# Optimization experiments

Hardware: AMD Instinct MI355X
Metric: run time of the kernel (lower is better)

The kernel has to match this reference:

```python
import jax, jax.numpy as jnp
import numpy as np
from jax import lax

B, C_IN, C_OUT, H, W, K, MID = 16, 256, 256, 64, 64, 3, 64
BN_EPS = 1e-5


def setup_inputs() -> dict:
    key = jax.random.key(0)
    ks = jax.random.split(key, 16)
    inp = {
        'x': jax.random.normal(ks[0], (B, C_IN, H, W), dtype=jnp.float32),
        # 4 kernel banks: (4, c2, c1//g, k, k)
        'weight': jax.random.normal(ks[1], (4, C_OUT, C_IN, K, K), dtype=jnp.float32) * 0.05,
        'gamma': jnp.ones((C_OUT,), jnp.float32),
        'beta': jnp.zeros((C_OUT,), jnp.float32),
    }
    # four attention branches: Linear(c, mid, bias=False) -> ReLU -> Linear(mid, 4, bias=True)
    names = ['s', 'c', 'f', 'w']
    for i, n in enumerate(names):
        inp[f'fc_{n}_w1'] = jax.random.normal(ks[2 + 3 * i], (MID, C_IN), dtype=jnp.float32) * 0.05
        inp[f'fc_{n}_w2'] = jax.random.normal(ks[3 + 3 * i], (4, MID), dtype=jnp.float32) * 0.05
        inp[f'fc_{n}_b2'] = jax.random.normal(ks[4 + 3 * i], (4,), dtype=jnp.float32) * 0.05
    return inp


def _branch(pooled, w1, w2, b2):
    # pooled: [B, C]; w1: [MID, C]; w2: [4, MID]
    h = jax.nn.relu(pooled @ w1.T)
    return jax.nn.softmax(h @ w2.T + b2, axis=1)  # [B, 4]


def reference(x, weight, gamma, beta,
              fc_s_w1, fc_s_w2, fc_s_b2,
              fc_c_w1, fc_c_w2, fc_c_b2,
              fc_f_w1, fc_f_w2, fc_f_b2,
              fc_w_w1, fc_w_w2, fc_w_b2):
    b = x.shape[0]
    pooled = jnp.mean(x, axis=(2, 3))  # GAP -> [B, C]
    alpha = (_branch(pooled, fc_s_w1, fc_s_w2, fc_s_b2)
             * _branch(pooled, fc_c_w1, fc_c_w2, fc_c_b2)
             * _branch(pooled, fc_f_w1, fc_f_w2, fc_f_b2)
             * _branch(pooled, fc_w_w1, fc_w_w2, fc_w_b2))  # [B, 4]
    # per-sample dynamic kernels: [B, out_c, in_c, k, k]
    dyn_w = jnp.einsum('bn,noikl->boikl', alpha, weight)

    def conv_one(xi, wi):
        # xi: [C, H, W]; wi: [out_c, in_c, k, k]
        return lax.conv_general_dilated(
            xi[None], wi, window_strides=(1, 1), padding='SAME',
            dimension_numbers=('NCHW', 'OIHW', 'NCHW'))[0]

    out = jax.vmap(conv_one)(x, dyn_w)  # [B, out_c, H, W]

    # BatchNorm2d (training-mode batch statistics)
    mean = jnp.mean(out, axis=(0, 2, 3))
    var = jnp.var(out, axis=(0, 2, 3))
    out = (out - mean[None, :, None, None]) * jax.lax.rsqrt(var + BN_EPS)[None, :, None, None]
    return out * gamma[None, :, None, None] + beta[None, :, None, None]
```

## Files before the change

kernel.cpp:

```cpp
#include <hip/hip_runtime.h>
#include <math.h>

#define BB 16
#define CIN 256
#define COUT 256
#define HH 64
#define WW 64
#define NBANK_STRIDE 589824

typedef short bf16x8 __attribute__((ext_vector_type(8)));
typedef float f32x4 __attribute__((ext_vector_type(4)));

#define WS_XT_OFF 32768
#define WS_DW_OFF 33587200
#define WS_NEED   52461568ULL

static __device__ __forceinline__ short f2bf(float f) {
    union { float f; unsigned u; } v; v.f = f;
    unsigned r = v.u + 0x7FFF + ((v.u >> 16) & 1);
    return (short)(r >> 16);
}

struct AttnParams {
    const float* w1[4];
    const float* w2[4];
    const float* b2[4];
};

__global__ __launch_bounds__(256) void xpose_kernel(const float* __restrict__ x,
                                                    short* __restrict__ xT,
                                                    float* __restrict__ pooled_part,
                                                    float* __restrict__ bn_part) {
    const int ci0 = blockIdx.x * 32;
    const int hg = blockIdx.y;
    const int h0 = hg * 4;
    const int b = blockIdx.z;
    const int t = threadIdx.x;
    if (blockIdx.x == 0 && hg == 0) bn_part[b * 256 + t] = 0.f;
    __shared__ __align__(16) short tile[2][64][40];
    const int ci = t >> 3;
    const int l = t & 7;
    const int w = t >> 2;
    const int s4 = t & 3;
    const float4* xrow = (const float4*)(x + ((size_t)(b * 256 + ci0 + ci)) * 4096 + h0 * 64);
    float sacc;
    {
        float4 v1 = xrow[l * 2];
        float4 v2 = xrow[l * 2 + 1];
        tile[0][l * 8 + 0][ci] = f2bf(v1.x);
        tile[0][l * 8 + 1][ci] = f2bf(v1.y);
        tile[0][l * 8 + 2][ci] = f2bf(v1.z);
        tile[0][l * 8 + 3][ci] = f2bf(v1.w);
        tile[0][l * 8 + 4][ci] = f2bf(v2.x);
        tile[0][l * 8 + 5][ci] = f2bf(v2.y);
        tile[0][l * 8 + 6][ci] = f2bf(v2.z);
        tile[0][l * 8 + 7][ci] = f2bf(v2.w);
        sacc = v1.x + v1.y + v1.z + v1.w + v2.x + v2.y + v2.z + v2.w;
    }
#pragma unroll
    for (int hh = 0; hh < 4; ++hh) {
        float4 nv1, nv2;
        if (hh < 3) {
            nv1 = xrow[(hh + 1) * 16 + l * 2];
            nv2 = xrow[(hh + 1) * 16 + l * 2 + 1];
        }
        __syncthreads();
        {
            bf16x8 val = *(const bf16x8*)&tile[hh & 1][w][s4 * 8];
            *(bf16x8*)&xT[((size_t)b * 4096 + (h0 + hh) * 64 + w) * 256 + ci0 + s4 * 8] = val;
        }
        if (hh < 3) {
            short* dst = &tile[(hh + 1) & 1][l * 8][ci];
            dst[0 * 40] = f2bf(nv1.x);
            dst[1 * 40] = f2bf(nv1.y);
            dst[2 * 40] = f2bf(nv1.z);
            dst[3 * 40] = f2bf(nv1.w);
            dst[4 * 40] = f2bf(nv2.x);
            dst[5 * 40] = f2bf(nv2.y);
            dst[6 * 40] = f2bf(nv2.z);
            dst[7 * 40] = f2bf(nv2.w);
            sacc += nv1.x + nv1.y + nv1.z + nv1.w + nv2.x + nv2.y + nv2.z + nv2.w;
        }
    }
    sacc += __shfl_xor(sacc, 1, 64);
    sacc += __shfl_xor(sacc, 2, 64);
    sacc += __shfl_xor(sacc, 4, 64);
    if (l == 0) pooled_part[((b * 16 + hg) << 8) + ci0 + ci] = sacc;
}

__global__ __launch_bounds__(256) void attn_kernel(AttnParams p,
                                                   const float* __restrict__ pooled_part,
                                                   float* __restrict__ ws_f) {
    const int b = blockIdx.x;
    const int t = threadIdx.x;
    const int wv = t >> 6;
    const int lane = t & 63;
    __shared__ float ps[256];
    __shared__ float hs[4][64];
    __shared__ float lg[4][4];
    __shared__ float sm[4][4];
    {
        float s = 0.f;
#pragma unroll
        for (int g = 0; g < 16; ++g) s += pooled_part[((b * 16 + g) << 8) + t];
        ps[t] = s * (1.0f / 4096.0f);
    }
    __syncthreads();
    {
        const float4* w1v = (const float4*)(p.w1[wv] + lane * 256);
        float h = 0.f;
#pragma unroll 8
        for (int i = 0; i < 64; ++i) {
            float4 w4 = w1v[i];
            h += w4.x * ps[i * 4 + 0] + w4.y * ps[i * 4 + 1] +
                 w4.z * ps[i * 4 + 2] + w4.w * ps[i * 4 + 3];
        }
        hs[wv][lane] = fmaxf(h, 0.f);
    }
    __syncthreads();
    if (t < 16) {
        const int n = t >> 2, j = t & 3;
        const float* w2 = p.w2[n];
        float l = p.b2[n][j];
        for (int m = 0; m < 64; ++m) l += w2[j * 64 + m] * hs[n][m];
        lg[n][j] = l;
    }
    __syncthreads();
    if (t < 4) {
        const int n = t;
        float mx = fmaxf(fmaxf(lg[n][0], lg[n][1]), fmaxf(lg[n][2], lg[n][3]));
        float e0 = expf(lg[n][0] - mx), e1 = expf(lg[n][1] - mx);
        float e2 = expf(lg[n][2] - mx), e3 = expf(lg[n][3] - mx);
        float inv = 1.f / (e0 + e1 + e2 + e3);
        sm[n][0] = e0 * inv; sm[n][1] = e1 * inv; sm[n][2] = e2 * inv; sm[n][3] = e3 * inv;
    }
    __syncthreads();
    if (t < 4) ws_f[b * 256 + t] = sm[0][t] * sm[1][t] * sm[2][t] * sm[3][t];
}

__global__ __launch_bounds__(256) void dynw_kernel(const float* __restrict__ wt,
                                                   const float* __restrict__ ws_f,
                                                   short* __restrict__ dynwF) {
    const int co = blockIdx.x;
    const int ci = threadIdx.x;
    const int cotile = co >> 4;
    const int mh = co & 15;
    __shared__ __align__(16) short st[9][272];
    float w[4][9];
#pragma unroll
    for (int n = 0; n < 4; ++n) {
        const size_t base = ((size_t)(n * 256 + co) * 256 + ci) * 9;
#pragma unroll
        for (int k = 0; k < 9; ++k) w[n][k] = wt[base + k];
    }
    for (int b = 0; b < BB; ++b) {
        const float a0 = ws_f[b * 256 + 0];
        const float a1 = ws_f[b * 256 + 1];
        const float a2 = ws_f[b * 256 + 2];
        const float a3 = ws_f[b * 256 + 3];
#pragma unroll
        for (int k = 0; k < 9; ++k)
            st[k][ci] = f2bf(a0 * w[0][k] + a1 * w[1][k] + a2 * w[2][k] + a3 * w[3][k]);
        __syncthreads();
#pragma unroll
        for (int i = 0; i < 2; ++i) {
            const int task = ci + 256 * i;
            if (task < 288) {
                const int k = task >> 5;
                const int c5 = task & 31;
                const int cc = c5 >> 2;
                const int q = c5 & 3;
                bf16x8 v = *(const bf16x8*)&st[k][cc * 32 + q * 8];
                *(bf16x8*)&dynwF[((size_t)((b * 9 + k) * 16 + cotile) << 12) + cc * 512 + q * 128 + mh * 8] = v;
            }
        }
        __syncthreads();
    }
}

__global__ __launch_bounds__(256, 2) void conv_mfma_kernel(const short* __restrict__ xT,
                                                           const short* __restrict__ dynwF,
                                                           float* __restrict__ out,
                                                           float* __restrict__ bn_part) {
    const int id = blockIdx.x;
    const int xcd = id & 7;
    const int wi = id >> 3;
    const int b = xcd + ((wi >> 5) << 3);
    const int rem = wi & 31;
    const int mt = rem >> 4;
    const int nt = rem & 15;

    const int t = threadIdx.x;
    const int lane = t & 63;
    const int wv = t >> 6;
    const int wx = wv & 1;
    const int wy = wv >> 1;
    const int mh = lane & 15;
    const int q = lane >> 4;
    const int r0 = nt * 4;
    const int co0 = mt * 128;

    __shared__ __align__(16) short xs[396 * 64];
    __shared__ __align__(16) short As[2][4096];
    __shared__ float red[128][2][2];

    f32x4 acc[4][8];
#pragma unroll
    for (int i = 0; i < 4; ++i)
#pragma unroll
        for (int j = 0; j < 8; ++j) acc[i][j] = (f32x4){0.f, 0.f, 0.f, 0.f};

    const size_t a_b9 = (size_t)b * 9;
    const int a_ct = mt * 8 + (t >> 5);
    const int a_port16 = (t & 31) * 16;
    const int a_dst = (t >> 5) * 512 + a_port16;
    const int a_rd0 = (wy * 4) * 512 + lane * 8;

    const bf16x8 zero8 = {0, 0, 0, 0, 0, 0, 0, 0};

    for (int cc = 0; cc < 8; ++cc) {
        const int ci0 = cc * 32;
        __syncthreads();
        const short* asrc0 = dynwF + ((((a_b9 + 0) * 16 + a_ct) * 8 + cc) << 9) + a_port16;
        bf16x8 pa0 = *(const bf16x8*)(asrc0);
        bf16x8 pa1 = *(const bf16x8*)(asrc0 + 8);
#pragma unroll
        for (int i = 0; i < 7; ++i) {
            int idx = t + 256 * i;
            if (idx < 1584) {
                int p = idx >> 2;
                int sub = idx & 3;
                int lr = p / 66;
                int lc = p - lr * 66;
                int r = r0 - 1 + lr;
                int c = lc - 1;
                bf16x8 v = zero8;
                if ((unsigned)r < 64u && (unsigned)c < 64u)
                    v = *(const bf16x8*)&xT[((size_t)b * 4096 + r * 64 + c) * 256 + ci0 + sub * 8];
                *(bf16x8*)&xs[(p << 6) + ((sub ^ (p & 7)) << 3)] = v;
            }
        }
        *(bf16x8*)&As[0][a_dst] = pa0;
        *(bf16x8*)&As[0][a_dst + 8] = pa1;
        __syncthreads();
#pragma unroll
        for (int khw = 0; khw < 9; ++khw) {
            const int kh = khw / 3;
            const int kw = khw - kh * 3;
            bf16x8 na0, na1;
            if (khw < 8) {
                const short* s = dynwF + ((((a_b9 + khw + 1) * 16 + a_ct) * 8 + cc) << 9) + a_port16;
                na0 = *(const bf16x8*)(s);
                na1 = *(const bf16x8*)(s + 8);
            }
            bf16x8 bfr[8];
#pragma unroll
            for (int ni = 0; ni < 8; ++ni) {
                const int row_l = wx * 2 + (ni >> 2) + kh;
                const int col_l = (ni & 3) * 16 + kw + mh;
                const int pp = row_l * 66 + col_l;
                bfr[ni] = *(const bf16x8*)&xs[(pp << 6) + ((q ^ (pp & 7)) << 3)];
            }
#pragma unroll
            for (int mi = 0; mi < 4; ++mi) {
                bf16x8 af = *(const bf16x8*)&As[khw & 1][a_rd0 + mi * 512];
#pragma unroll
                for (int ni = 0; ni < 8; ++ni)
                    acc[mi][ni] = __builtin_amdgcn_mfma_f32_16x16x32_bf16(af, bfr[ni], acc[mi][ni], 0, 0, 0);
            }
            if (khw < 8) {
                *(bf16x8*)&As[(khw + 1) & 1][a_dst] = na0;
                *(bf16x8*)&As[(khw + 1) & 1][a_dst + 8] = na1;
                __syncthreads();
            }
        }
    }

    float s16[4][4], q16[4][4];
#pragma unroll
    for (int mi = 0; mi < 4; ++mi)
#pragma unroll
        for (int reg = 0; reg < 4; ++reg) { s16[mi][reg] = 0.f; q16[mi][reg] = 0.f; }

#pragma unroll
    for (int mi = 0; mi < 4; ++mi) {
#pragma unroll
        for (int ni = 0; ni < 8; ++ni) {
            const int pix = wx * 128 + ni * 16 + mh;
            const int h = r0 + (pix >> 6);
            const int w = pix & 63;
#pragma unroll
            for (int reg = 0; reg < 4; ++reg) {
                const int co = co0 + wy * 64 + mi * 16 + q * 4 + reg;
                const float e = acc[mi][ni][reg];
                out[(((size_t)b * 256 + co) << 12) + (h << 6) + w] = e;
                s16[mi][reg] += e;
                q16[mi][reg] += e * e;
            }
        }
    }
#pragma unroll
    for (int mi = 0; mi < 4; ++mi)
#pragma unroll
        for (int reg = 0; reg < 4; ++reg) {
            float s = s16[mi][reg], sq = q16[mi][reg];
            s += __shfl_xor(s, 1, 64);  sq += __shfl_xor(sq, 1, 64);
            s += __shfl_xor(s, 2, 64);  sq += __shfl_xor(sq, 2, 64);
            s += __shfl_xor(s, 4, 64);  sq += __shfl_xor(sq, 4, 64);
            s += __shfl_xor(s, 8, 64);  sq += __shfl_xor(sq, 8, 64);
            if (mh == 0) {
                const int co_l = wy * 64 + mi * 16 + q * 4 + reg;
                red[co_l][0][wx] = s;
                red[co_l][1][wx] = sq;
            }
        }
    __syncthreads();
    {
        const int co_l = t >> 1;
        const int st = t & 1;
        float v = red[co_l][st][0] + red[co_l][st][1];
        atomicAdd(&bn_part[(st * 256 + co0 + co_l) * 8 + (nt & 7)], v);
    }
}

__global__ __launch_bounds__(256) void bn_apply_kernel(float* __restrict__ out,
                                                       const float* __restrict__ bn_part,
                                                       const float* __restrict__ gamma,
                                                       const float* __restrict__ beta) {
    const int gid = blockIdx.x * 256 + threadIdx.x;
    const int c = (blockIdx.x >> 2) & 255;
    float S = 0.f, Q = 0.f;
#pragma unroll
    for (int s = 0; s < 8; ++s) {
        S += bn_part[c * 8 + s];
        Q += bn_part[(256 + c) * 8 + s];
    }
    const float mean = S * (1.f / 65536.f);
    const float var = Q * (1.f / 65536.f) - mean * mean;
    const float inv = rsqrtf(var + 1e-5f);
    const float sc = gamma[c] * inv;
    const float sh = beta[c] - mean * sc;
    float4* p = (float4*)out;
    float4 v = p[gid];
    v.x = v.x * sc + sh;
    v.y = v.y * sc + sh;
    v.z = v.z * sc + sh;
    v.w = v.w * sc + sh;
    p[gid] = v;
}

__global__ __launch_bounds__(256) void gap_kernel(const float* __restrict__ x,
                                                  float* __restrict__ pooled) {
    const int plane = blockIdx.x;
    const float4* p = (const float4*)(x + (size_t)plane * 4096);
    const int t = threadIdx.x;
    float s = 0.f;
#pragma unroll
    for (int i = 0; i < 4; ++i) {
        float4 v = p[t + 256 * i];
        s += v.x + v.y + v.z + v.w;
    }
#pragma unroll
    for (int off = 32; off > 0; off >>= 1) s += __shfl_down(s, off, 64);
    __shared__ float red[4];
    if ((t & 63) == 0) red[t >> 6] = s;
    __syncthreads();
    if (t == 0) pooled[plane] = (red[0] + red[1] + red[2] + red[3]) * (1.0f / 4096.0f);
}

__global__ __launch_bounds__(64) void attn64_kernel(const float* __restrict__ pooled,
                                                    AttnParams p,
                                                    float* __restrict__ alpha) {
    const int b = blockIdx.x;
    const int t = threadIdx.x;
    __shared__ float ps[256];
    __shared__ float hs[64];
    __shared__ float lg[4];
    __shared__ float prod[4];
#pragma unroll
    for (int i = 0; i < 4; ++i) ps[t + 64 * i] = pooled[b * 256 + t + 64 * i];
    if (t < 4) prod[t] = 1.f;
    __syncthreads();
    for (int n = 0; n < 4; ++n) {
        const float* w1 = p.w1[n];
        float h = 0.f;
        for (int c = 0; c < 256; ++c) h += w1[t * 256 + c] * ps[c];
        hs[t] = fmaxf(h, 0.f);
        __syncthreads();
        if (t < 4) {
            const float* w2 = p.w2[n];
            float l = p.b2[n][t];
            for (int m = 0; m < 64; ++m) l += w2[t * 64 + m] * hs[m];
            lg[t] = l;
        }
        __syncthreads();
        if (t == 0) {
            float mx = fmaxf(fmaxf(lg[0], lg[1]), fmaxf(lg[2], lg[3]));
            float e0 = expf(lg[0] - mx), e1 = expf(lg[1] - mx);
            float e2 = expf(lg[2] - mx), e3 = expf(lg[3] - mx);
            float inv = 1.f / (e0 + e1 + e2 + e3);
            prod[0] *= e0 * inv; prod[1] *= e1 * inv;
            prod[2] *= e2 * inv; prod[3] *= e3 * inv;
        }
        __syncthreads();
    }
    if (t < 4) alpha[b * 4 + t] = prod[t];
}

__global__ __launch_bounds__(256) void conv_fp32_kernel(const float* __restrict__ x,
                                                        const float* __restrict__ wt,
                                                        const float* __restrict__ alpha,
                                                        float* __restrict__ out) {
    const int h = blockIdx.x;
    const int cot = blockIdx.y;
    const int b = blockIdx.z;
    const int t = threadIdx.x;
    const int tx = t & 15;
    const int ty = t >> 4;
    const int co0 = cot * 64;
    __shared__ __align__(16) float xsf[32][68];
    __shared__ __align__(16) float wshf[3][32][68];
    const float a0 = alpha[b * 4 + 0], a1 = alpha[b * 4 + 1];
    const float a2 = alpha[b * 4 + 2], a3 = alpha[b * 4 + 3];
    float acc[4][4];
#pragma unroll
    for (int i = 0; i < 4; ++i)
#pragma unroll
        for (int j = 0; j < 4; ++j) acc[i][j] = 0.f;
    const size_t xbase = (size_t)b * CIN * 4096;
    for (int kh = 0; kh < 3; ++kh) {
        const int r = h + kh - 1;
        if (r < 0 || r >= HH) continue;
        for (int chunk = 0; chunk < 8; ++chunk) {
            const int ci0 = chunk * 32;
            __syncthreads();
#pragma unroll
            for (int i = 0; i < 8; ++i) {
                int flat = t + 256 * i;
                int ci = flat >> 6;
                int w = flat & 63;
                xsf[ci][1 + w] = x[xbase + (size_t)(ci0 + ci) * 4096 + r * 64 + w];
            }
            if (t < 32) { xsf[t][0] = 0.f; xsf[t][65] = 0.f; xsf[t][66] = 0.f; xsf[t][67] = 0.f; }
#pragma unroll
            for (int j = 0; j < 24; ++j) {
                int e = t + 256 * j;
                int co = e / 96;
                int rem = e - co * 96;
                int ci = rem / 3;
                int kw = rem - ci * 3;
                size_t g = (((size_t)(co0 + co) * 256 + (ci0 + ci)) * 3 + kh) * 3 + kw;
                wshf[kw][ci][co] = a0 * wt[g] + a1 * wt[g + NBANK_STRIDE] +
                                   a2 * wt[g + 2 * NBANK_STRIDE] + a3 * wt[g + 3 * NBANK_STRIDE];
            }
            __syncthreads();
            for (int ci = 0; ci < 32; ++ci) {
                float4 w0 = *(const float4*)&wshf[0][ci][tx * 4];
                float4 w1v = *(const float4*)&wshf[1][ci][tx * 4];
                float4 w2v = *(const float4*)&wshf[2][ci][tx * 4];
                float4 xa = *(const float4*)&xsf[ci][ty * 4];
                float4 xb = *(const float4*)&xsf[ci][ty * 4 + 4];
                float v[8] = {xa.x, xa.y, xa.z, xa.w, xb.x, xb.y, xb.z, xb.w};
                float aw[3][4] = {{w0.x, w0.y, w0.z, w0.w},
                                  {w1v.x, w1v.y, w1v.z, w1v.w},
                                  {w2v.x, w2v.y, w2v.z, w2v.w}};
#pragma unroll
                for (int kw = 0; kw < 3; ++kw)
#pragma unroll
                    for (int i = 0; i < 4; ++i)
#pragma unroll
                        for (int j = 0; j < 4; ++j)
                            acc[i][j] += aw[kw][i] * v[j + kw];
            }
        }
    }
    size_t obase = (((size_t)b * COUT + co0 + tx * 4) * 64 + h) * 64 + ty * 4;
#pragma unroll
    for (int i = 0; i < 4; ++i) {
        float4 o = {acc[i][0], acc[i][1], acc[i][2], acc[i][3]};
        *(float4*)&out[obase + (size_t)i * 4096] = o;
    }
}

__global__ __launch_bounds__(256) void bn_stats_kernel(const float* __restrict__ out,
                                                       const float* __restrict__ gamma,
                                                       const float* __restrict__ beta,
                                                       float* __restrict__ scale,
                                                       float* __restrict__ shift) {
    const int co = blockIdx.x;
    const int t = threadIdx.x;
    float s = 0.f, sq = 0.f;
    for (int b = 0; b < BB; ++b) {
        const float4* p = (const float4*)(out + ((size_t)b * 256 + co) * 4096);
#pragma unroll
        for (int i = 0; i < 4; ++i) {
            float4 v = p[t + 256 * i];
            s += v.x + v.y + v.z + v.w;
            sq += v.x * v.x + v.y * v.y + v.z * v.z + v.w * v.w;
        }
    }
#pragma unroll
    for (int off = 32; off > 0; off >>= 1) {
        s += __shfl_down(s, off, 64);
        sq += __shfl_down(sq, off, 64);
    }
    __shared__ float rs[4], rq[4];
    if ((t & 63) == 0) { rs[t >> 6] = s; rq[t >> 6] = sq; }
    __syncthreads();
    if (t == 0) {
        float S = rs[0] + rs[1] + rs[2] + rs[3];
        float Q = rq[0] + rq[1] + rq[2] + rq[3];
        float mean = S * (1.f / 65536.f);
        float var = Q * (1.f / 65536.f) - mean * mean;
        float inv = rsqrtf(var + 1e-5f);
        float sc = gamma[co] * inv;
        scale[co] = sc;
        shift[co] = beta[co] - mean * sc;
    }
}

__global__ __launch_bounds__(256) void bn_apply_sc_kernel(float* __restrict__ out,
                                                          const float* __restrict__ scale,
                                                          const float* __restrict__ shift) {
    const int gid = blockIdx.x * 256 + threadIdx.x;
    const int c = (gid >> 10) & 255;
    float4* p = (float4*)out;
    float4 v = p[gid];
    const float sc = scale[c], sh = shift[c];
    v.x = v.x * sc + sh;
    v.y = v.y * sc + sh;
    v.z = v.z * sc + sh;
    v.w = v.w * sc + sh;
    p[gid] = v;
}

extern "C" void kernel_launch(void* const* d_in, const int* in_sizes, int n_in,
                              void* d_out, int out_size, void* d_ws, size_t ws_size,
                              hipStream_t stream) {
    (void)in_sizes; (void)n_in; (void)out_size;
    const float* x = (const float*)d_in[0];
    const float* wt = (const float*)d_in[1];
    const float* gamma = (const float*)d_in[2];
    const float* beta = (const float*)d_in[3];
    AttnParams ap;
    for (int n = 0; n < 4; ++n) {
        ap.w1[n] = (const float*)d_in[4 + 3 * n];
        ap.w2[n] = (const float*)d_in[5 + 3 * n];
        ap.b2[n] = (const float*)d_in[6 + 3 * n];
    }
    float* ws_f = (float*)d_ws;
    float* out = (float*)d_out;

    if (ws_size >= WS_NEED) {
        short* xT = (short*)((char*)d_ws + WS_XT_OFF);
        short* dynwF = (short*)((char*)d_ws + WS_DW_OFF);
        float* pooled_part = (float*)((char*)d_ws + WS_DW_OFF);
        float* bn_part = ws_f + 4096;

        xpose_kernel<<<dim3(8, 16, 16), 256, 0, stream>>>(x, xT, pooled_part, bn_part);
        attn_kernel<<<16, 256, 0, stream>>>(ap, pooled_part, ws_f);
        dynw_kernel<<<256, 256, 0, stream>>>(wt, ws_f, dynwF);
        conv_mfma_kernel<<<512, 256, 0, stream>>>(xT, dynwF, out, bn_part);
        bn_apply_kernel<<<16384, 256, 0, stream>>>(out, bn_part, gamma, beta);
    } else {
        float* pooled = ws_f;
        float* alpha = ws_f + 4096;
        float* scale = ws_f + 4160;
        float* shift = ws_f + 4416;
        gap_kernel<<<4096, 256, 0, stream>>>(x, pooled);
        attn64_kernel<<<16, 64, 0, stream>>>(pooled, ap, alpha);
        conv_fp32_kernel<<<dim3(64, 4, 16), 256, 0, stream>>>(x, wt, alpha, out);
        bn_stats_kernel<<<256, 256, 0, stream>>>(out, gamma, beta, scale, shift);
        bn_apply_sc_kernel<<<16384, 256, 0, stream>>>(out, scale, shift);
    }
}
```

Measured before the change: 269.6 us.

## Fuse attention MLP into dynamic-weight kernel and split batch across grid

Merges the attention kernel into the dynamic-weight kernel: each block recomputes the attention coefficients for its four batch samples (one wavefront per sample) and then builds the bf16 dynamic weights for those samples. The grid grows from 256 to 256x4 blocks, each handling four samples instead of sixteen. This removes one launch and the serial dependency on a tiny 16-block kernel, and adds parallelism to the weight build. The cost is redundant recomputation of the attention MLP in every block and reloading the bank weights four times. The pooled partial sums are now staged in the output buffer rather than a separate workspace region.

```diff
diff --git a/kernel.cpp b/kernel.cpp
--- a/kernel.cpp
+++ b/kernel.cpp
@@ -88,83 +88,85 @@
     if (l == 0) pooled_part[((b * 16 + hg) << 8) + ci0 + ci] = sacc;
 }
 
-__global__ __launch_bounds__(256) void attn_kernel(AttnParams p,
-                                                   const float* __restrict__ pooled_part,
-                                                   float* __restrict__ ws_f) {
-    const int b = blockIdx.x;
+__global__ __launch_bounds__(256) void dynw_attn_kernel(const float* __restrict__ wt,
+                                                        const float* __restrict__ pp,
+                                                        AttnParams p,
+                                                        short* __restrict__ dynwF) {
+    const int co = blockIdx.x;
+    const int bg = blockIdx.y;
     const int t = threadIdx.x;
     const int wv = t >> 6;
     const int lane = t & 63;
-    __shared__ float ps[256];
-    __shared__ float hs[4][64];
-    __shared__ float lg[4][4];
-    __shared__ float sm[4][4];
-    {
+    const int cotile = co >> 4;
+    const int mh = co & 15;
+    __shared__ __align__(16) short st[9][272];
+    __shared__ float psL[4][256];
+    __shared__ float hsL[4][4][64];
+    __shared__ float lgL[4][4][4];
+    __shared__ float smL[4][4][4];
+    __shared__ float alL[4][4];
+
+    float w[4][9];
+#pragma unroll
+    for (int n = 0; n < 4; ++n) {
+        const size_t base = ((size_t)(n * 256 + co) * 256 + t) * 9;
+#pragma unroll
+        for (int k = 0; k < 9; ++k) w[n][k] = wt[base + k];
+    }
+
+    const int b_at = bg * 4 + wv;
+#pragma unroll
+    for (int j = 0; j < 4; ++j) {
+        const int c = j * 64 + lane;
         float s = 0.f;
 #pragma unroll
-        for (int g = 0; g < 16; ++g) s += pooled_part[((b * 16 + g) << 8) + t];
-        ps[t] = s * (1.0f / 4096.0f);
-    }
-    __syncthreads();
-    {
-        const float4* w1v = (const float4*)(p.w1[wv] + lane * 256);
+        for (int g = 0; g < 16; ++g) s += pp[((b_at * 16 + g) << 8) + c];
+        psL[wv][c] = s * (1.0f / 4096.0f);
+    }
+#pragma unroll
+    for (int n = 0; n < 4; ++n) {
+        const float4* w1v = (const float4*)(p.w1[n] + lane * 256);
         float h = 0.f;
 #pragma unroll 8
         for (int i = 0; i < 64; ++i) {
             float4 w4 = w1v[i];
-            h += w4.x * ps[i * 4 + 0] + w4.y * ps[i * 4 + 1] +
-                 w4.z * ps[i * 4 + 2] + w4.w * ps[i * 4 + 3];
-        }
-        hs[wv][lane] = fmaxf(h, 0.f);
-    }
-    __syncthreads();
-    if (t < 16) {
-        const int n = t >> 2, j = t & 3;
+            h += w4.x * psL[wv][i * 4 + 0] + w4.y * psL[wv][i * 4 + 1] +
+                 w4.z * psL[wv][i * 4 + 2] + w4.w * psL[wv][i * 4 + 3];
+        }
+        hsL[wv][n][lane] = fmaxf(h, 0.f);
+    }
+    if (lane < 16) {
+        const int n = lane >> 2, j = lane & 3;
         const float* w2 = p.w2[n];
         float l = p.b2[n][j];
-        for (int m = 0; m < 64; ++m) l += w2[j * 64 + m] * hs[n][m];
-        lg[n][j] = l;
+        for (int m = 0; m < 64; ++m) l += w2[j * 64 + m] * hsL[wv][n][m];
+        lgL[wv][n][j] = l;
+    }
+    if (lane < 4) {
+        const int n = lane;
+        float mx = fmaxf(fmaxf(lgL[wv][n][0], lgL[wv][n][1]), fmaxf(lgL[wv][n][2], lgL[wv][n][3]));
+        float e0 = expf(lgL[wv][n][0] - mx), e1 = expf(lgL[wv][n][1] - mx);
+        float e2 = expf(lgL[wv][n][2] - mx), e3 = expf(lgL[wv][n][3] - mx);
+        float inv = 1.f / (e0 + e1 + e2 + e3);
+        smL[wv][n][0] = e0 * inv; smL[wv][n][1] = e1 * inv;
+        smL[wv][n][2] = e2 * inv; smL[wv][n][3] = e3 * inv;
+    }
+    if (lane < 4) {
+        const int j = lane;
+        alL[wv][j] = smL[wv][0][j] * smL[wv][1][j] * smL[wv][2][j] * smL[wv][3][j];
     }
     __syncthreads();
-    if (t < 4) {
-        const int n = t;
-        float mx = fmaxf(fmaxf(lg[n][0], lg[n][1]), fmaxf(lg[n][2], lg[n][3]));
-        float e0 = expf(lg[n][0] - mx), e1 = expf(lg[n][1] - mx);
-        float e2 = expf(lg[n][2] - mx), e3 = expf(lg[n][3] - mx);
-        float inv = 1.f / (e0 + e1 + e2 + e3);
-        sm[n][0] = e0 * inv; sm[n][1] = e1 * inv; sm[n][2] = e2 * inv; sm[n][3] = e3 * inv;
-    }
-    __syncthreads();
-    if (t < 4) ws_f[b * 256 + t] = sm[0][t] * sm[1][t] * sm[2][t] * sm[3][t];
-}
-
-__global__ __launch_bounds__(256) void dynw_kernel(const float* __restrict__ wt,
-                                                   const float* __restrict__ ws_f,
-                                                   short* __restrict__ dynwF) {
-    const int co = blockIdx.x;
-    const int ci = threadIdx.x;
-    const int cotile = co >> 4;
-    const int mh = co & 15;
-    __shared__ __align__(16) short st[9][272];
-    float w[4][9];
-#pragma unroll
-    for (int n = 0; n < 4; ++n) {
-        const size_t base = ((size_t)(n * 256 + co) * 256 + ci) * 9;
-#pragma unroll
-        for (int k = 0; k < 9; ++k) w[n][k] = wt[base + k];
-    }
-    for (int b = 0; b < BB; ++b) {
-        const float a0 = ws_f[b * 256 + 0];
-        const float a1 = ws_f[b * 256 + 1];
-        const float a2 = ws_f[b * 256 + 2];
-        const float a3 = ws_f[b * 256 + 3];
+
+    for (int bb = 0; bb < 4; ++bb) {
+        const float a0 = alL[bb][0], a1 = alL[bb][1], a2 = alL[bb][2], a3 = alL[bb][3];
 #pragma unroll
         for (int k = 0; k < 9; ++k)
-            st[k][ci] = f2bf(a0 * w[0][k] + a1 * w[1][k] + a2 * w[2][k] + a3 * w[3][k]);
-        __syncthreads();
+            st[k][t] = f2bf(a0 * w[0][k] + a1 * w[1][k] + a2 * w[2][k] + a3 * w[3][k]);
+        __syncthreads();
+        const int b = bg * 4 + bb;
 #pragma unroll
         for (int i = 0; i < 2; ++i) {
-            const int task = ci + 256 * i;
+            const int task = t + 256 * i;
             if (task < 288) {
                 const int k = task >> 5;
                 const int c5 = task & 31;
@@ -554,12 +556,11 @@
     if (ws_size >= WS_NEED) {
         short* xT = (short*)((char*)d_ws + WS_XT_OFF);
         short* dynwF = (short*)((char*)d_ws + WS_DW_OFF);
-        float* pooled_part = (float*)((char*)d_ws + WS_DW_OFF);
+        float* pooled_part = out;
         float* bn_part = ws_f + 4096;
 
         xpose_kernel<<<dim3(8, 16, 16), 256, 0, stream>>>(x, xT, pooled_part, bn_part);
-        attn_kernel<<<16, 256, 0, stream>>>(ap, pooled_part, ws_f);
-        dynw_kernel<<<256, 256, 0, stream>>>(wt, ws_f, dynwF);
+        dynw_attn_kernel<<<dim3(256, 4), 256, 0, stream>>>(wt, pooled_part, ap, dynwF);
         conv_mfma_kernel<<<512, 256, 0, stream>>>(xT, dynwF, out, bn_part);
         bn_apply_kernel<<<16384, 256, 0, stream>>>(out, bn_part, gamma, beta);
     } else {
```

Measured after the change: 366.4 us. +35.9%, slower.
